# Optimization experiments

Measured on AMD Instinct MI355X. Metric: run time of the kernel, lower is better.

The kernel has to match this reference:

```python
import jax, jax.numpy as jnp
import numpy as np

N_P, N_D = 100000, 50000
C, S, H = 128, 128, 128
E = 600000


def setup_inputs() -> dict:
    key = jax.random.key(0)
    ks = jax.random.split(key, 20)
    sc = 1.0 / np.sqrt(H)
    inp = {
        "h_p": jax.random.normal(ks[0], (N_P, C), dtype=jnp.float32),
        "h_d": jax.random.normal(ks[1], (N_D, S), dtype=jnp.float32),
        "pd_src": jax.random.randint(ks[2], (E,), 0, N_P),
        "pd_dst": jax.random.randint(ks[3], (E,), 0, N_D),
        "dp_src": jax.random.randint(ks[4], (E,), 0, N_D),
        "dp_dst": jax.random.randint(ks[5], (E,), 0, N_P),
    }
    names = [("W1_pd", (C, H)), ("W1_dp", (S, H)), ("W2_pd", (H, H)),
             ("W2_dp", (H, H)), ("W3_pd", (H, S)), ("W3_dp", (H, C))]
    for i, (nm, shp) in enumerate(names):
        inp[nm] = jax.random.normal(ks[6 + i], shp, dtype=jnp.float32) * sc
        inp["b" + nm[1:]] = jnp.zeros((shp[1],), dtype=jnp.float32)
    return inp


def gconv(x, src, dst, n_dst, W, b):
    """DGL GraphConv, norm='both': relu(D_dst^-1/2 A D_src^-1/2 X W + b)."""
    n_src = x.shape[0]
    ones = jnp.ones(src.shape, dtype=x.dtype)
    deg_out = jnp.maximum(jax.ops.segment_sum(ones, src, num_segments=n_src), 1.0)
    deg_in = jnp.maximum(jax.ops.segment_sum(ones, dst, num_segments=n_dst), 1.0)
    xs = x * jax.lax.rsqrt(deg_out)[:, None]
    m = jax.ops.segment_sum(xs[src], dst, num_segments=n_dst)  # [n_dst, d_in]
    m = m * jax.lax.rsqrt(deg_in)[:, None]
    return jax.nn.relu(m @ W + b)


def reference(h_p, h_d, pd_src, pd_dst, dp_src, dp_dst,
              W1_pd, b1_pd, W1_dp, b1_dp,
              W2_pd, b2_pd, W2_dp, b2_dp,
              W3_pd, b3_pd, W3_dp, b3_dp):
    # Layer 1: p_d sends p feats to d; d_p sends d feats to p
    h_d1 = gconv(h_p, pd_src, pd_dst, N_D, W1_pd, b1_pd)
    h_p1 = gconv(h_d, dp_src, dp_dst, N_P, W1_dp, b1_dp)
    # Layer 2
    h_d2 = gconv(h_p1, pd_src, pd_dst, N_D, W2_pd, b2_pd)
    h_p2 = gconv(h_d1, dp_src, dp_dst, N_P, W2_dp, b2_dp)
    # Layer 3: d gets S-dim, p gets C-dim
    h_d3 = gconv(h_p2, pd_src, pd_dst, N_D, W3_pd, b3_pd)
    h_p3 = gconv(h_d2, dp_src, dp_dst, N_P, W3_dp, b3_dp)
    return h_p3, h_d3
```

## Files before the change

### kernel.cpp

```cpp
#include <hip/hip_runtime.h>
#include <stdint.h>

#define N_P 100000
#define N_D 50000
#define NE  600000
#define F   128
#define FP  136

#define NCHK   32
#define CHKE   18752
#define HPARTS 8
#define HPART_P (N_P/HPARTS)
#define HPART_D (N_D/HPARTS)
#define HOFS_A0 ((size_t)0)
#define HOFS_A1 ((size_t)32*N_P)
#define HOFS_A2 ((size_t)32*N_P + (size_t)32*N_D)
#define HOFS_A3 ((size_t)32*N_P + (size_t)64*N_D)

typedef __attribute__((ext_vector_type(8))) __bf16 bf16x8;
typedef __attribute__((ext_vector_type(4))) float  f32x4;

static __device__ __forceinline__ float bf2f(uint16_t u){
  union{float f;uint32_t i;} v; v.i = ((uint32_t)u)<<16; return v.f;
}
static __device__ __forceinline__ uint16_t f2bf(float f){
  union{float f;uint32_t i;} v; v.f = f;
  uint32_t i = v.i;
  uint32_t r = i + 0x7fffu + ((i>>16)&1u);
  return (uint16_t)(r>>16);
}

__global__ __launch_bounds__(256) void k_hist(
    const int* __restrict__ pd_src, const int* __restrict__ pd_dst,
    const int* __restrict__ dp_src, const int* __restrict__ dp_dst,
    int* __restrict__ hist){
  __shared__ int cnt[HPART_P];
  const int b = blockIdx.x;
  const int arr = b >> 8, part = (b >> 5) & 7, chunk = b & 31;
  const int* src; int N; size_t hofs;
  switch(arr){
    case 0:  src = pd_src; N = N_P; hofs = HOFS_A0; break;
    case 1:  src = pd_dst; N = N_D; hofs = HOFS_A1; break;
    case 2:  src = dp_src; N = N_D; hofs = HOFS_A2; break;
    default: src = dp_dst; N = N_P; hofs = HOFS_A3; break;
  }
  const int PART = N / HPARTS;
  const int lo = part * PART;
  for (int i = threadIdx.x; i < PART; i += 256) cnt[i] = 0;
  __syncthreads();
  const int e0 = chunk*CHKE, e1 = min(e0 + CHKE, NE);
  const uint4* s4 = (const uint4*)(src + e0);
  const int n4 = (e1 - e0) >> 2;
  for (int i = threadIdx.x; i < n4; i += 256){
    uint4 v = s4[i];
    int a0 = (int)v.x - lo, a1 = (int)v.y - lo, a2 = (int)v.z - lo, a3 = (int)v.w - lo;
    if ((unsigned)a0 < (unsigned)PART) atomicAdd(&cnt[a0], 1);
    if ((unsigned)a1 < (unsigned)PART) atomicAdd(&cnt[a1], 1);
    if ((unsigned)a2 < (unsigned)PART) atomicAdd(&cnt[a2], 1);
    if ((unsigned)a3 < (unsigned)PART) atomicAdd(&cnt[a3], 1);
  }
  __syncthreads();
  int* out = hist + hofs + (size_t)chunk*N + lo;
  for (int i = threadIdx.x; i < PART; i += 256) out[i] = cnt[i];
}

__global__ void k_sumdeg(int* __restrict__ hist,
                         int* __restrict__ cnt_d_in, int* __restrict__ cnt_p_in,
                         float* __restrict__ rs_p_out, float* __restrict__ rs_p_in,
                         float* __restrict__ rs_d_out, float* __restrict__ rs_d_in){
  const int idx = blockIdx.x*256 + threadIdx.x;
  const int arr = blockIdx.y;
  int N; size_t hofs; bool pre;
  switch(arr){
    case 0:  N = N_P; hofs = HOFS_A0; pre = false; break;
    case 1:  N = N_D; hofs = HOFS_A1; pre = true;  break;
    case 2:  N = N_D; hofs = HOFS_A2; pre = false; break;
    default: N = N_P; hofs = HOFS_A3; pre = true;  break;
  }
  if (idx >= N) return;
  int* base = hist + hofs + idx;
  int run = 0;
  if (pre){
    #pragma unroll 4
    for (int c = 0; c < NCHK; ++c){
      int v = base[(size_t)c*N]; base[(size_t)c*N] = run; run += v;
    }
  } else {
    #pragma unroll 4
    for (int c = 0; c < NCHK; ++c) run += base[(size_t)c*N];
  }
  float rs = rsqrtf((float)max(run, 1));
  switch(arr){
    case 0:  rs_p_out[idx] = rs; break;
    case 1:  cnt_d_in[idx] = run; rs_d_in[idx] = rs; break;
    case 2:  rs_d_out[idx] = rs; break;
    default: cnt_p_in[idx] = run; rs_p_in[idx] = rs; break;
  }
}

__global__ void k_scan1(const int* __restrict__ cA, int nA,
                        const int* __restrict__ cB, int nB,
                        int* __restrict__ bsums, int nbA){
  __shared__ int red[8];
  int b = blockIdx.x, t = threadIdx.x;
  const int* in; int n, bi, slot;
  if (b < nbA){ in = cA; n = nA; bi = b;       slot = bi; }
  else        { in = cB; n = nB; bi = b - nbA; slot = 256 + bi; }
  int i = bi*512 + t;
  int v = (i < n) ? in[i] : 0;
  #pragma unroll
  for (int o = 32; o; o >>= 1) v += __shfl_down(v, o, 64);
  if ((t & 63) == 0) red[t >> 6] = v;
  __syncthreads();
  if (t == 0){ int s = 0; for (int k = 0; k < 8; ++k) s += red[k]; bsums[slot] = s; }
}

__global__ void k_scan2(int* bsums, int nbA, int nbB){
  __shared__ int sh[256];
  int seg = blockIdx.x, t = threadIdx.x;
  int nb = seg ? nbB : nbA;
  int* p = bsums + seg*256;
  int v = (t < nb) ? p[t] : 0;
  sh[t] = v; __syncthreads();
  for (int ofs = 1; ofs < 256; ofs <<= 1){
    int u = (t >= ofs) ? sh[t-ofs] : 0; __syncthreads();
    sh[t] += u; __syncthreads();
  }
  if (t < nb) p[t] = sh[t] - v;
}

__global__ void k_scan3(const int* __restrict__ cA, int nA,
                        const int* __restrict__ cB, int nB,
                        const int* __restrict__ bsums, int nbA,
                        int* __restrict__ offA, int* __restrict__ offB){
  __shared__ int sh[512];
  int b = blockIdx.x, t = threadIdx.x;
  const int* in; int n, bi; int* out; int base;
  if (b < nbA){ in = cA; n = nA; bi = b;       out = offA; base = bsums[bi]; }
  else        { in = cB; n = nB; bi = b - nbA; out = offB; base = bsums[256+bi]; }
  int i = bi*512 + t;
  int v = (i < n) ? in[i] : 0;
  sh[t] = v; __syncthreads();
  for (int ofs = 1; ofs < 512; ofs <<= 1){
    int u = (t >= ofs) ? sh[t-ofs] : 0; __syncthreads();
    sh[t] += u; __syncthreads();
  }
  if (i < n) out[i] = base + sh[t] - v;
  if (b == 0 && t == 0){ offA[nA] = NE; offB[nB] = NE; }
}

__global__ __launch_bounds__(256) void k_scatter(
    const int* __restrict__ pd_src, const int* __restrict__ pd_dst,
    const int* __restrict__ dp_src, const int* __restrict__ dp_dst,
    const int* __restrict__ off_pd, const int* __restrict__ off_dp,
    const int* __restrict__ hist,
    int* __restrict__ col_pd, int* __restrict__ col_dp){
  __shared__ int base[HPART_P];
  const int b = blockIdx.x;
  const int gph = b >> 8, part = (b >> 5) & 7, chunk = b & 31;
  const int* dsts; const int* srcs; const int* off; int* col; int N; size_t hofs;
  if (gph == 0){ dsts = pd_dst; srcs = pd_src; off = off_pd; col = col_pd; N = N_D; hofs = HOFS_A1; }
  else         { dsts = dp_dst; srcs = dp_src; off = off_dp; col = col_dp; N = N_P; hofs = HOFS_A3; }
  const int PART = N / HPARTS;
  const int lo = part * PART;
  const int* hc   = hist + hofs + (size_t)chunk*N + lo;
  const int* offp = off + lo;
  for (int i = threadIdx.x; i < PART; i += 256) base[i] = offp[i] + hc[i];
  __syncthreads();
  const int e0 = chunk*CHKE, e1 = min(e0 + CHKE, NE);
  const uint4* d4 = (const uint4*)(dsts + e0);
  const int n4 = (e1 - e0) >> 2;
  for (int i = threadIdx.x; i < n4; i += 256){
    uint4 d = d4[i];
    int a0 = (int)d.x - lo, a1 = (int)d.y - lo, a2 = (int)d.z - lo, a3 = (int)d.w - lo;
    int e = e0 + 4*i;
    if ((unsigned)a0 < (unsigned)PART){ int p = atomicAdd(&base[a0], 1); col[p] = srcs[e+0]; }
    if ((unsigned)a1 < (unsigned)PART){ int p = atomicAdd(&base[a1], 1); col[p] = srcs[e+1]; }
    if ((unsigned)a2 < (unsigned)PART){ int p = atomicAdd(&base[a2], 1); col[p] = srcs[e+2]; }
    if ((unsigned)a3 < (unsigned)PART){ int p = atomicAdd(&base[a3], 1); col[p] = srcs[e+3]; }
  }
}

__global__ void k_convert(const float4* __restrict__ hp, const float4* __restrict__ hd,
                          const float* __restrict__ rs_po, const float* __restrict__ rs_do,
                          uint2* __restrict__ P0, uint2* __restrict__ D0,
                          const float* w0,const float* w1,const float* w2,
                          const float* w3,const float* w4,const float* w5,
                          uint16_t* __restrict__ wt,
                          uint16_t* z0, uint16_t* z1, uint16_t* z2,
                          uint16_t* z3, uint16_t* z4, uint16_t* z5){
  if (blockIdx.x < 6){
    int m = blockIdx.x;
    const float* W; uint16_t* Z;
    switch(m){ case 0:W=w0;Z=z0;break; case 1:W=w1;Z=z1;break; case 2:W=w2;Z=z2;break;
               case 3:W=w3;Z=z3;break; case 4:W=w4;Z=z4;break; default:W=w5;Z=z5; }
    uint16_t* T = wt + m*F*FP;
    for (int idx = threadIdx.x; idx < F*F; idx += 256){
      int k = idx >> 7, j = idx & 127;
      T[j*FP + k] = f2bf(W[idx]);
    }
    if (threadIdx.x < F) Z[threadIdx.x] = 0;
    return;
  }
  int i = (blockIdx.x - 6)*256 + threadIdx.x;
  const int nP4 = N_P*F/4, nD4 = N_D*F/4;
  if (i < nP4){
    float4 v = hp[i]; float s = rs_po[i >> 5];
    uint2 r;
    r.x = ((uint32_t)f2bf(v.y*s)<<16) | f2bf(v.x*s);
    r.y = ((uint32_t)f2bf(v.w*s)<<16) | f2bf(v.z*s);
    P0[i] = r;
  } else {
    int j = i - nP4;
    if (j < nD4){
      float4 v = hd[j]; float s = rs_do[j >> 5];
      uint2 r;
      r.x = ((uint32_t)f2bf(v.y*s)<<16) | f2bf(v.x*s);
      r.y = ((uint32_t)f2bf(v.w*s)<<16) | f2bf(v.z*s);
      D0[j] = r;
    }
  }
}

template<int OUT_MODE>
__global__ __launch_bounds__(256, 4) void k_gconv2(
    const uint16_t* __restrict__ xA, const int* __restrict__ offAp, const int* __restrict__ colA,
    const float* __restrict__ rsA, const uint16_t* __restrict__ WtA, const float* __restrict__ biasA,
    const float* __restrict__ rsnA, void* __restrict__ outA, int ndA, int nsA, int nblkA,
    const uint16_t* __restrict__ xB, const int* __restrict__ offBp, const int* __restrict__ colB,
    const float* __restrict__ rsB, const uint16_t* __restrict__ WtB, const float* __restrict__ biasB,
    const float* __restrict__ rsnB, void* __restrict__ outB, int ndB, int nsB)
{
  __shared__ uint16_t m_lds[64*FP];
  const int tid  = threadIdx.x;
  const int lane = tid & 63;
  const int wv   = tid >> 6;

  const uint16_t* x; const int* off; const int* col; const float* rs_in;
  const uint16_t* Wt; const float* bias; const float* rs_next; void* outp;
  int n_dst, zrow, bid;
  if ((int)blockIdx.x < nblkA){
    x = xA; off = offAp; col = colA; rs_in = rsA; Wt = WtA; bias = biasA;
    rs_next = rsnA; outp = outA; n_dst = ndA; zrow = nsA; bid = blockIdx.x;
  } else {
    x = xB; off = offBp; col = colB; rs_in = rsB; Wt = WtB; bias = biasB;
    rs_next = rsnB; outp = outB; n_dst = ndB; zrow = nsB; bid = blockIdx.x - nblkA;
  }

  const int row0 = bid*64 + wv*16;
  const int g    = lane >> 4;
  const int l    = lane & 15;
  const uint16_t* xl = x + l*8;

  int e0a[4], e1a[4], cva[4];
  #pragma unroll
  for (int i = 0; i < 4; ++i){
    int r = row0 + i*4 + g;
    bool rv = r < n_dst;
    e0a[i] = rv ? off[r]   : 0;
    e1a[i] = rv ? off[r+1] : 0;
  }
  #pragma unroll
  for (int i = 0; i < 4; ++i){
    int last = (e1a[i] > 0) ? e1a[i]-1 : 0;
    int idx  = e0a[i] + l;
    cva[i] = col[idx < e1a[i] ? idx : last];
  }

  #pragma unroll
  for (int i = 0; i < 4; ++i){
    int e0 = e0a[i], e1 = e1a[i];
    int cv = cva[i];
    float a0=0.f,a1=0.f,a2=0.f,a3=0.f,a4=0.f,a5=0.f,a6=0.f,a7=0.f;
    for (int e = e0; e < e1; e += 16){
      int nidx = e + 16 + l;
      int ncv  = col[nidx < e1 ? nidx : e1-1];
      int cnt  = e1 - e;
      const bool more = (cnt > 8);
      int cb[16];
      #pragma unroll
      for (int q = 0; q < 8; ++q) cb[q] = __shfl(cv, g*16 + q, 64);
      if (more){
        #pragma unroll
        for (int q = 8; q < 16; ++q) cb[q] = __shfl(cv, g*16 + q, 64);
      }
      uint4 u[8], w[8];
      #pragma unroll
      for (int q = 0; q < 8; ++q){
        int c = (q < cnt) ? cb[q] : zrow;
        u[q] = *(const uint4*)(xl + (size_t)c*F);
      }
      if (more){
        #pragma unroll
        for (int q = 8; q < 16; ++q){
          int c = (q < cnt) ? cb[q] : zrow;
          w[q-8] = *(const uint4*)(xl + (size_t)c*F);
        }
      }
      #pragma unroll
      for (int q = 0; q < 8; ++q){
        a0 += bf2f((uint16_t)u[q].x); a1 += bf2f((uint16_t)(u[q].x>>16));
        a2 += bf2f((uint16_t)u[q].y); a3 += bf2f((uint16_t)(u[q].y>>16));
        a4 += bf2f((uint16_t)u[q].z); a5 += bf2f((uint16_t)(u[q].z>>16));
        a6 += bf2f((uint16_t)u[q].w); a7 += bf2f((uint16_t)(u[q].w>>16));
      }
      if (more){
        #pragma unroll
        for (int q = 0; q < 8; ++q){
          a0 += bf2f((uint16_t)w[q].x); a1 += bf2f((uint16_t)(w[q].x>>16));
          a2 += bf2f((uint16_t)w[q].y); a3 += bf2f((uint16_t)(w[q].y>>16));
          a4 += bf2f((uint16_t)w[q].z); a5 += bf2f((uint16_t)(w[q].z>>16));
          a6 += bf2f((uint16_t)w[q].w); a7 += bf2f((uint16_t)(w[q].w>>16));
        }
      }
      cv = ncv;
    }
    int r = row0 + i*4 + g;
    float rs = (r < n_dst) ? rs_in[r] : 0.f;
    uint4 pk;
    pk.x = ((uint32_t)f2bf(a1*rs)<<16) | f2bf(a0*rs);
    pk.y = ((uint32_t)f2bf(a3*rs)<<16) | f2bf(a2*rs);
    pk.z = ((uint32_t)f2bf(a5*rs)<<16) | f2bf(a4*rs);
    pk.w = ((uint32_t)f2bf(a7*rs)<<16) | f2bf(a6*rs);
    *(uint4*)&m_lds[(wv*16 + i*4 + g)*FP + l*8] = pk;
  }

  f32x4 acc[8];
  #pragma unroll
  for (int t = 0; t < 8; ++t) acc[t] = (f32x4){0.f,0.f,0.f,0.f};
  const int mrow = lane & 15;
  const int kgrp = lane >> 4;
  #pragma unroll
  for (int k0 = 0; k0 < F; k0 += 32){
    bf16x8 bfrag = *(const bf16x8*)&m_lds[(wv*16 + mrow)*FP + k0 + kgrp*8];
    #pragma unroll
    for (int t = 0; t < 8; ++t){
      bf16x8 afrag = *(const bf16x8*)&Wt[(t*16 + mrow)*FP + k0 + kgrp*8];
      acc[t] = __builtin_amdgcn_mfma_f32_16x16x32_bf16(afrag, bfrag, acc[t], 0, 0, 0);
    }
  }

  const int q4 = kgrp * 4;
  const int rr = row0 + mrow;
  if (rr < n_dst){
    float rsn = (OUT_MODE == 0) ? rs_next[rr] : 1.f;
    #pragma unroll
    for (int t = 0; t < 8; ++t){
      float4 b4 = *(const float4*)&bias[t*16 + q4];
      float v0 = fmaxf(acc[t][0] + b4.x, 0.f);
      float v1 = fmaxf(acc[t][1] + b4.y, 0.f);
      float v2 = fmaxf(acc[t][2] + b4.z, 0.f);
      float v3 = fmaxf(acc[t][3] + b4.w, 0.f);
      if (OUT_MODE == 0){
        uint2 pk;
        pk.x = ((uint32_t)f2bf(v1*rsn)<<16) | f2bf(v0*rsn);
        pk.y = ((uint32_t)f2bf(v3*rsn)<<16) | f2bf(v2*rsn);
        *(uint2*)((uint16_t*)outp + (size_t)rr*F + t*16 + q4) = pk;
      } else {
        float4 o; o.x = v0; o.y = v1; o.z = v2; o.w = v3;
        *(float4*)((float*)outp + (size_t)rr*F + t*16 + q4) = o;
      }
    }
  }
}

extern "C" void kernel_launch(void* const* d_in, const int* in_sizes, int n_in,
                              void* d_out, int out_size, void* d_ws, size_t ws_size,
                              hipStream_t stream) {
  const float* h_p   = (const float*)d_in[0];
  const float* h_d   = (const float*)d_in[1];
  const int* pd_src  = (const int*)d_in[2];
  const int* pd_dst  = (const int*)d_in[3];
  const int* dp_src  = (const int*)d_in[4];
  const int* dp_dst  = (const int*)d_in[5];
  const float* W1_pd = (const float*)d_in[6];   const float* b1_pd = (const float*)d_in[7];
  const float* W1_dp = (const float*)d_in[8];   const float* b1_dp = (const float*)d_in[9];
  const float* W2_pd = (const float*)d_in[10];  const float* b2_pd = (const float*)d_in[11];
  const float* W2_dp = (const float*)d_in[12];  const float* b2_dp = (const float*)d_in[13];
  const float* W3_pd = (const float*)d_in[14];  const float* b3_pd = (const float*)d_in[15];
  const float* W3_dp = (const float*)d_in[16];  const float* b3_dp = (const float*)d_in[17];

  char* w = (char*)d_ws;
  size_t o = 0;
  auto take = [&](size_t bytes)->char*{
    char* p = w + o; o += (bytes + 255) & ~(size_t)255; return p;
  };

  int* cnt_d_in  = (int*)take(4*(size_t)N_D);
  int* cnt_p_in  = (int*)take(4*(size_t)N_P);
  int* off_pd   = (int*)take(4*(size_t)(N_D+1));
  int* off_dp   = (int*)take(4*(size_t)(N_P+1));
  int* bsums    = (int*)take(4*512);
  int* col_pd   = (int*)take(4*(size_t)NE);
  int* col_dp   = (int*)take(4*(size_t)NE);
  float* rs_p_out = (float*)take(4*(size_t)N_P);
  float* rs_p_in  = (float*)take(4*(size_t)N_P);
  float* rs_d_out = (float*)take(4*(size_t)N_D);
  float* rs_d_in  = (float*)take(4*(size_t)N_D);
  uint16_t* wt  = (uint16_t*)take(2*(size_t)6*F*FP);
  uint16_t* P0  = (uint16_t*)take(2*(size_t)(N_P+1)*F);
  uint16_t* P1  = (uint16_t*)take(2*(size_t)(N_P+1)*F);
  uint16_t* P2  = (uint16_t*)take(2*(size_t)(N_P+1)*F);
  uint16_t* D0  = (uint16_t*)take(2*(size_t)(N_D+1)*F);
  uint16_t* D1  = (uint16_t*)take(2*(size_t)(N_D+1)*F);
  uint16_t* D2  = (uint16_t*)take(2*(size_t)(N_D+1)*F);

  int* hist = (int*)P1;

  k_hist<<<4*HPARTS*NCHK, 256, 0, stream>>>(pd_src, pd_dst, dp_src, dp_dst, hist);
  k_sumdeg<<<dim3((N_P+255)/256, 4), 256, 0, stream>>>(
      hist, cnt_d_in, cnt_p_in, rs_p_out, rs_p_in, rs_d_out, rs_d_in);
  const int nbA = (N_D + 511)/512;
  const int nbB = (N_P + 511)/512;
  k_scan1<<<nbA+nbB, 512, 0, stream>>>(cnt_d_in, N_D, cnt_p_in, N_P, bsums, nbA);
  k_scan2<<<2, 256, 0, stream>>>(bsums, nbA, nbB);
  k_scan3<<<nbA+nbB, 512, 0, stream>>>(cnt_d_in, N_D, cnt_p_in, N_P, bsums, nbA, off_pd, off_dp);
  k_scatter<<<2*HPARTS*NCHK, 256, 0, stream>>>(pd_src, pd_dst, dp_src, dp_dst,
                                               off_pd, off_dp, hist, col_pd, col_dp);
  k_convert<<<((N_P+N_D)*F/4 + 255)/256 + 6, 256, 0, stream>>>(
      (const float4*)h_p, (const float4*)h_d, rs_p_out, rs_d_out, (uint2*)P0, (uint2*)D0,
      W1_pd, W1_dp, W2_pd, W2_dp, W3_pd, W3_dp, wt,
      P0 + (size_t)N_P*F, D0 + (size_t)N_D*F,
      P1 + (size_t)N_P*F, D1 + (size_t)N_D*F,
      P2 + (size_t)N_P*F, D2 + (size_t)N_D*F);

  const int gd = (N_D + 63)/64, gp = (N_P + 63)/64;
  k_gconv2<0><<<gd+gp, 256, 0, stream>>>(
      P0, off_pd, col_pd, rs_d_in, wt + 0*F*FP, b1_pd, rs_d_out, D1, N_D, N_P, gd,
      D0, off_dp, col_dp, rs_p_in, wt + 1*F*FP, b1_dp, rs_p_out, P1, N_P, N_D);
  k_gconv2<0><<<gd+gp, 256, 0, stream>>>(
      P1, off_pd, col_pd, rs_d_in, wt + 2*F*FP, b2_pd, rs_d_out, D2, N_D, N_P, gd,
      D1, off_dp, col_dp, rs_p_in, wt + 3*F*FP, b2_dp, rs_p_out, P2, N_P, N_D);
  k_gconv2<1><<<gd+gp, 256, 0, stream>>>(
      P2, off_pd, col_pd, rs_d_in, wt + 4*F*FP, b3_pd, nullptr, (float*)d_out + (size_t)N_P*F, N_D, N_P, gd,
      D2, off_dp, col_dp, rs_p_in, wt + 5*F*FP, b3_dp, nullptr, (float*)d_out, N_P, N_D);
}
```

Before: 465.8 us.

## Interleave two destination rows with software-pipelined 8-edge gather chunks

Restructures the gather-aggregate loop so that two destination rows are processed at once. Each row works through 8-edge chunks, and the loads for the next chunk are issued before the current chunk is accumulated. This is meant to raise memory-level parallelism and hide gather latency, since the old loop loaded and consumed each 16-edge chunk serially. The cost is more registers (two sets of 8 uint4 buffers plus accumulators), which could lower occupancy, and rows with uneven degree leave some iterations doing work for only one of the pair.

```diff
diff --git a/kernel.cpp b/kernel.cpp
--- a/kernel.cpp
+++ b/kernel.cpp
@@ -250,6 +250,7 @@
   const int row0 = bid*64 + wv*16;
   const int g    = lane >> 4;
   const int l    = lane & 15;
+  const int l8   = lane & 7;
   const uint16_t* xl = x + l*8;
 
   int e0a[4], e1a[4], cva[4];
@@ -262,67 +263,98 @@
   }
   #pragma unroll
   for (int i = 0; i < 4; ++i){
-    int last = (e1a[i] > 0) ? e1a[i]-1 : 0;
-    int idx  = e0a[i] + l;
-    cva[i] = col[idx < e1a[i] ? idx : last];
-  }
-
-  #pragma unroll
-  for (int i = 0; i < 4; ++i){
-    int e0 = e0a[i], e1 = e1a[i];
-    int cv = cva[i];
-    float a0=0.f,a1=0.f,a2=0.f,a3=0.f,a4=0.f,a5=0.f,a6=0.f,a7=0.f;
-    for (int e = e0; e < e1; e += 16){
-      int nidx = e + 16 + l;
-      int ncv  = col[nidx < e1 ? nidx : e1-1];
-      int cnt  = e1 - e;
-      const bool more = (cnt > 8);
-      int cb[16];
-      #pragma unroll
-      for (int q = 0; q < 8; ++q) cb[q] = __shfl(cv, g*16 + q, 64);
-      if (more){
+    int idx = e0a[i] + l8;
+    cva[i] = col[idx < e1a[i] ? idx : (e1a[i] > 0 ? e1a[i]-1 : 0)];
+  }
+
+  #pragma unroll
+  for (int pr = 0; pr < 2; ++pr){
+    const int iA = 2*pr, iB = 2*pr + 1;
+    int eA = e0a[iA]; const int e1A = e1a[iA];
+    int eB = e0a[iB]; const int e1B = e1a[iB];
+    int cvA = cva[iA], cvB = cva[iB];
+    float aA[8], aB[8];
+    #pragma unroll
+    for (int q = 0; q < 8; ++q){ aA[q] = 0.f; aB[q] = 0.f; }
+    uint4 uA[8], uB[8];
+
+    int cntA = e1A - eA; cntA = cntA > 8 ? 8 : (cntA < 0 ? 0 : cntA);
+    #pragma unroll
+    for (int q = 0; q < 8; ++q){
+      int c = (q < cntA) ? __shfl(cvA, g*16 + q, 64) : zrow;
+      uA[q] = *(const uint4*)(xl + (size_t)c*F);
+    }
+    { int nidx = eA + 8 + l8; cvA = col[nidx < e1A ? nidx : (e1A > 0 ? e1A-1 : 0)]; }
+
+    int cntB = e1B - eB; cntB = cntB > 8 ? 8 : (cntB < 0 ? 0 : cntB);
+    #pragma unroll
+    for (int q = 0; q < 8; ++q){
+      int c = (q < cntB) ? __shfl(cvB, g*16 + q, 64) : zrow;
+      uB[q] = *(const uint4*)(xl + (size_t)c*F);
+    }
+    { int nidx = eB + 8 + l8; cvB = col[nidx < e1B ? nidx : (e1B > 0 ? e1B-1 : 0)]; }
+
+    while (cntA | cntB){
+      if (cntA){
         #pragma unroll
-        for (int q = 8; q < 16; ++q) cb[q] = __shfl(cv, g*16 + q, 64);
-      }
-      uint4 u[8], w[8];
-      #pragma unroll
-      for (int q = 0; q < 8; ++q){
-        int c = (q < cnt) ? cb[q] : zrow;
-        u[q] = *(const uint4*)(xl + (size_t)c*F);
-      }
-      if (more){
-        #pragma unroll
-        for (int q = 8; q < 16; ++q){
-          int c = (q < cnt) ? cb[q] : zrow;
-          w[q-8] = *(const uint4*)(xl + (size_t)c*F);
+        for (int q = 0; q < 8; ++q){
+          aA[0] += bf2f((uint16_t)uA[q].x); aA[1] += bf2f((uint16_t)(uA[q].x>>16));
+          aA[2] += bf2f((uint16_t)uA[q].y); aA[3] += bf2f((uint16_t)(uA[q].y>>16));
+          aA[4] += bf2f((uint16_t)uA[q].z); aA[5] += bf2f((uint16_t)(uA[q].z>>16));
+          aA[6] += bf2f((uint16_t)uA[q].w); aA[7] += bf2f((uint16_t)(uA[q].w>>16));
+        }
+        eA += cntA;
+        cntA = e1A - eA; cntA = cntA > 8 ? 8 : (cntA < 0 ? 0 : cntA);
+        if (cntA){
+          #pragma unroll
+          for (int q = 0; q < 8; ++q){
+            int c = (q < cntA) ? __shfl(cvA, g*16 + q, 64) : zrow;
+            uA[q] = *(const uint4*)(xl + (size_t)c*F);
+          }
+          int nidx = eA + 8 + l8; cvA = col[nidx < e1A ? nidx : e1A-1];
         }
       }
-      #pragma unroll
-      for (int q = 0; q < 8; ++q){
-        a0 += bf2f((uint16_t)u[q].x); a1 += bf2f((uint16_t)(u[q].x>>16));
-        a2 += bf2f((uint16_t)u[q].y); a3 += bf2f((uint16_t)(u[q].y>>16));
-        a4 += bf2f((uint16_t)u[q].z); a5 += bf2f((uint16_t)(u[q].z>>16));
-        a6 += bf2f((uint16_t)u[q].w); a7 += bf2f((uint16_t)(u[q].w>>16));
-      }
-      if (more){
+      if (cntB){
         #pragma unroll
         for (int q = 0; q < 8; ++q){
-          a0 += bf2f((uint16_t)w[q].x); a1 += bf2f((uint16_t)(w[q].x>>16));
-          a2 += bf2f((uint16_t)w[q].y); a3 += bf2f((uint16_t)(w[q].y>>16));
-          a4 += bf2f((uint16_t)w[q].z); a5 += bf2f((uint16_t)(w[q].z>>16));
-          a6 += bf2f((uint16_t)w[q].w); a7 += bf2f((uint16_t)(w[q].w>>16));
+          aB[0] += bf2f((uint16_t)uB[q].x); aB[1] += bf2f((uint16_t)(uB[q].x>>16));
+          aB[2] += bf2f((uint16_t)uB[q].y); aB[3] += bf2f((uint16_t)(uB[q].y>>16));
+          aB[4] += bf2f((uint16_t)uB[q].z); aB[5] += bf2f((uint16_t)(uB[q].z>>16));
+          aB[6] += bf2f((uint16_t)uB[q].w); aB[7] += bf2f((uint16_t)(uB[q].w>>16));
+        }
+        eB += cntB;
+        cntB = e1B - eB; cntB = cntB > 8 ? 8 : (cntB < 0 ? 0 : cntB);
+        if (cntB){
+          #pragma unroll
+          for (int q = 0; q < 8; ++q){
+            int c = (q < cntB) ? __shfl(cvB, g*16 + q, 64) : zrow;
+            uB[q] = *(const uint4*)(xl + (size_t)c*F);
+          }
+          int nidx = eB + 8 + l8; cvB = col[nidx < e1B ? nidx : e1B-1];
         }
       }
-      cv = ncv;
-    }
-    int r = row0 + i*4 + g;
-    float rs = (r < n_dst) ? rs_in[r] : 0.f;
-    uint4 pk;
-    pk.x = ((uint32_t)f2bf(a1*rs)<<16) | f2bf(a0*rs);
-    pk.y = ((uint32_t)f2bf(a3*rs)<<16) | f2bf(a2*rs);
-    pk.z = ((uint32_t)f2bf(a5*rs)<<16) | f2bf(a4*rs);
-    pk.w = ((uint32_t)f2bf(a7*rs)<<16) | f2bf(a6*rs);
-    *(uint4*)&m_lds[(wv*16 + i*4 + g)*FP + l*8] = pk;
+    }
+
+    {
+      int r = row0 + iA*4 + g;
+      float rs = (r < n_dst) ? rs_in[r] : 0.f;
+      uint4 pk;
+      pk.x = ((uint32_t)f2bf(aA[1]*rs)<<16) | f2bf(aA[0]*rs);
+      pk.y = ((uint32_t)f2bf(aA[3]*rs)<<16) | f2bf(aA[2]*rs);
+      pk.z = ((uint32_t)f2bf(aA[5]*rs)<<16) | f2bf(aA[4]*rs);
+      pk.w = ((uint32_t)f2bf(aA[7]*rs)<<16) | f2bf(aA[6]*rs);
+      *(uint4*)&m_lds[(wv*16 + iA*4 + g)*FP + l*8] = pk;
+    }
+    {
+      int r = row0 + iB*4 + g;
+      float rs = (r < n_dst) ? rs_in[r] : 0.f;
+      uint4 pk;
+      pk.x = ((uint32_t)f2bf(aB[1]*rs)<<16) | f2bf(aB[0]*rs);
+      pk.y = ((uint32_t)f2bf(aB[3]*rs)<<16) | f2bf(aB[2]*rs);
+      pk.z = ((uint32_t)f2bf(aB[5]*rs)<<16) | f2bf(aB[4]*rs);
+      pk.w = ((uint32_t)f2bf(aB[7]*rs)<<16) | f2bf(aB[6]*rs);
+      *(uint4*)&m_lds[(wv*16 + iB*4 + g)*FP + l*8] = pk;
+    }
   }
 
   f32x4 acc[8];
```

New measurement: 514.3 us. 10.4% more time.

## Replace chunked LDS histogram CSR build with global-atomic degree count and scatter

Applied to the files above, without the earlier changes.

Degree counting now uses direct global atomics on zeroed degree arrays instead of per-chunk shared-memory histograms plus a column-summing pass, and the rsqrt normalisation moves into the first scan kernel. The CSR scatter likewise uses global atomic cursors initialised by the scan rather than per-block LDS bases from the histogram. This removes the large histogram buffer traffic and the many redundant edge re-reads per partition, at the cost of global atomic contention and a non-deterministic edge order within each row.

```diff
diff --git a/kernel.cpp b/kernel.cpp
--- a/kernel.cpp
+++ b/kernel.cpp
@@ -7,16 +7,6 @@
 #define F   128
 #define FP  136
 
-#define NCHK   32
-#define CHKE   18752
-#define HPARTS 8
-#define HPART_P (N_P/HPARTS)
-#define HPART_D (N_D/HPARTS)
-#define HOFS_A0 ((size_t)0)
-#define HOFS_A1 ((size_t)32*N_P)
-#define HOFS_A2 ((size_t)32*N_P + (size_t)32*N_D)
-#define HOFS_A3 ((size_t)32*N_P + (size_t)64*N_D)
-
 typedef __attribute__((ext_vector_type(8))) __bf16 bf16x8;
 typedef __attribute__((ext_vector_type(4))) float  f32x4;
 
@@ -30,89 +20,54 @@
   return (uint16_t)(r>>16);
 }
 
-__global__ __launch_bounds__(256) void k_hist(
+__global__ __launch_bounds__(256) void k_deg(
     const int* __restrict__ pd_src, const int* __restrict__ pd_dst,
     const int* __restrict__ dp_src, const int* __restrict__ dp_dst,
-    int* __restrict__ hist){
-  __shared__ int cnt[HPART_P];
-  const int b = blockIdx.x;
-  const int arr = b >> 8, part = (b >> 5) & 7, chunk = b & 31;
-  const int* src; int N; size_t hofs;
+    int* __restrict__ deg_p_out, int* __restrict__ deg_d_in,
+    int* __restrict__ deg_d_out, int* __restrict__ deg_p_in){
+  const int n4 = NE/4;
+  int i = blockIdx.x*256 + threadIdx.x;
+  if (i >= 4*n4) return;
+  const int arr = i / n4;
+  const int j   = i - arr*n4;
+  const uint4* s4; int* deg;
   switch(arr){
-    case 0:  src = pd_src; N = N_P; hofs = HOFS_A0; break;
-    case 1:  src = pd_dst; N = N_D; hofs = HOFS_A1; break;
-    case 2:  src = dp_src; N = N_D; hofs = HOFS_A2; break;
-    default: src = dp_dst; N = N_P; hofs = HOFS_A3; break;
-  }
-  const int PART = N / HPARTS;
-  const int lo = part * PART;
-  for (int i = threadIdx.x; i < PART; i += 256) cnt[i] = 0;
-  __syncthreads();
-  const int e0 = chunk*CHKE, e1 = min(e0 + CHKE, NE);
-  const uint4* s4 = (const uint4*)(src + e0);
-  const int n4 = (e1 - e0) >> 2;
-  for (int i = threadIdx.x; i < n4; i += 256){
-    uint4 v = s4[i];
-    int a0 = (int)v.x - lo, a1 = (int)v.y - lo, a2 = (int)v.z - lo, a3 = (int)v.w - lo;
-    if ((unsigned)a0 < (unsigned)PART) atomicAdd(&cnt[a0], 1);
-    if ((unsigned)a1 < (unsigned)PART) atomicAdd(&cnt[a1], 1);
-    if ((unsigned)a2 < (unsigned)PART) atomicAdd(&cnt[a2], 1);
-    if ((unsigned)a3 < (unsigned)PART) atomicAdd(&cnt[a3], 1);
-  }
-  __syncthreads();
-  int* out = hist + hofs + (size_t)chunk*N + lo;
-  for (int i = threadIdx.x; i < PART; i += 256) out[i] = cnt[i];
-}
-
-__global__ void k_sumdeg(int* __restrict__ hist,
-                         int* __restrict__ cnt_d_in, int* __restrict__ cnt_p_in,
-                         float* __restrict__ rs_p_out, float* __restrict__ rs_p_in,
-                         float* __restrict__ rs_d_out, float* __restrict__ rs_d_in){
-  const int idx = blockIdx.x*256 + threadIdx.x;
-  const int arr = blockIdx.y;
-  int N; size_t hofs; bool pre;
-  switch(arr){
-    case 0:  N = N_P; hofs = HOFS_A0; pre = false; break;
-    case 1:  N = N_D; hofs = HOFS_A1; pre = true;  break;
-    case 2:  N = N_D; hofs = HOFS_A2; pre = false; break;
-    default: N = N_P; hofs = HOFS_A3; pre = true;  break;
-  }
-  if (idx >= N) return;
-  int* base = hist + hofs + idx;
-  int run = 0;
-  if (pre){
-    #pragma unroll 4
-    for (int c = 0; c < NCHK; ++c){
-      int v = base[(size_t)c*N]; base[(size_t)c*N] = run; run += v;
-    }
-  } else {
-    #pragma unroll 4
-    for (int c = 0; c < NCHK; ++c) run += base[(size_t)c*N];
-  }
-  float rs = rsqrtf((float)max(run, 1));
-  switch(arr){
-    case 0:  rs_p_out[idx] = rs; break;
-    case 1:  cnt_d_in[idx] = run; rs_d_in[idx] = rs; break;
-    case 2:  rs_d_out[idx] = rs; break;
-    default: cnt_p_in[idx] = run; rs_p_in[idx] = rs; break;
-  }
+    case 0:  s4 = (const uint4*)pd_src; deg = deg_p_out; break;
+    case 1:  s4 = (const uint4*)pd_dst; deg = deg_d_in;  break;
+    case 2:  s4 = (const uint4*)dp_src; deg = deg_d_out; break;
+    default: s4 = (const uint4*)dp_dst; deg = deg_p_in;  break;
+  }
+  uint4 v = s4[j];
+  atomicAdd(&deg[v.x], 1);
+  atomicAdd(&deg[v.y], 1);
+  atomicAdd(&deg[v.z], 1);
+  atomicAdd(&deg[v.w], 1);
 }
 
 __global__ void k_scan1(const int* __restrict__ cA, int nA,
                         const int* __restrict__ cB, int nB,
-                        int* __restrict__ bsums, int nbA){
+                        int* __restrict__ bsums, int nbA,
+                        const int* __restrict__ oA, const int* __restrict__ oB,
+                        float* __restrict__ riA, float* __restrict__ roA,
+                        float* __restrict__ riB, float* __restrict__ roB){
   __shared__ int red[8];
   int b = blockIdx.x, t = threadIdx.x;
-  const int* in; int n, bi, slot;
-  if (b < nbA){ in = cA; n = nA; bi = b;       slot = bi; }
-  else        { in = cB; n = nB; bi = b - nbA; slot = 256 + bi; }
+  const int* in; const int* od; float* ri; float* ro; int n, bi, slot;
+  if (b < nbA){ in = cA; od = oA; ri = riA; ro = roA; n = nA; bi = b;       slot = bi; }
+  else        { in = cB; od = oB; ri = riB; ro = roB; n = nB; bi = b - nbA; slot = 256 + bi; }
   int i = bi*512 + t;
-  int v = (i < n) ? in[i] : 0;
-  #pragma unroll
-  for (int o = 32; o; o >>= 1) v += __shfl_down(v, o, 64);
-  if ((t & 63) == 0) red[t >> 6] = v;
+  int v = 0;
+  if (i < n){
+    v = in[i];
+    ri[i] = rsqrtf((float)max(v, 1));
+    ro[i] = rsqrtf((float)max(od[i], 1));
+  }
+  int s = v;
+  #pragma unroll
+  for (int o = 32; o; o >>= 1) s += __shfl_down(s, o, 64);
+  if ((t & 63) == 0) red[t >> 6] = s;
   __syncthreads();
-  if (t == 0){ int s = 0; for (int k = 0; k < 8; ++k) s += red[k]; bsums[slot] = s; }
+  if (t == 0){ int acc = 0; for (int k = 0; k < 8; ++k) acc += red[k]; bsums[slot] = acc; }
 }
 
 __global__ void k_scan2(int* bsums, int nbA, int nbB){
@@ -132,12 +87,13 @@
 __global__ void k_scan3(const int* __restrict__ cA, int nA,
                         const int* __restrict__ cB, int nB,
                         const int* __restrict__ bsums, int nbA,
-                        int* __restrict__ offA, int* __restrict__ offB){
+                        int* __restrict__ offA, int* __restrict__ offB,
+                        int* __restrict__ curA, int* __restrict__ curB){
   __shared__ int sh[512];
   int b = blockIdx.x, t = threadIdx.x;
-  const int* in; int n, bi; int* out; int base;
-  if (b < nbA){ in = cA; n = nA; bi = b;       out = offA; base = bsums[bi]; }
-  else        { in = cB; n = nB; bi = b - nbA; out = offB; base = bsums[256+bi]; }
+  const int* in; int n, bi; int* out; int* cur; int base;
+  if (b < nbA){ in = cA; n = nA; bi = b;       out = offA; cur = curA; base = bsums[bi]; }
+  else        { in = cB; n = nB; bi = b - nbA; out = offB; cur = curB; base = bsums[256+bi]; }
   int i = bi*512 + t;
   int v = (i < n) ? in[i] : 0;
   sh[t] = v; __syncthreads();
@@ -145,40 +101,28 @@
     int u = (t >= ofs) ? sh[t-ofs] : 0; __syncthreads();
     sh[t] += u; __syncthreads();
   }
-  if (i < n) out[i] = base + sh[t] - v;
+  if (i < n){ int val = base + sh[t] - v; out[i] = val; cur[i] = val; }
   if (b == 0 && t == 0){ offA[nA] = NE; offB[nB] = NE; }
 }
 
-__global__ __launch_bounds__(256) void k_scatter(
+__global__ __launch_bounds__(256) void k_scatter2(
     const int* __restrict__ pd_src, const int* __restrict__ pd_dst,
     const int* __restrict__ dp_src, const int* __restrict__ dp_dst,
-    const int* __restrict__ off_pd, const int* __restrict__ off_dp,
-    const int* __restrict__ hist,
+    int* __restrict__ cur_pd, int* __restrict__ cur_dp,
     int* __restrict__ col_pd, int* __restrict__ col_dp){
-  __shared__ int base[HPART_P];
-  const int b = blockIdx.x;
-  const int gph = b >> 8, part = (b >> 5) & 7, chunk = b & 31;
-  const int* dsts; const int* srcs; const int* off; int* col; int N; size_t hofs;
-  if (gph == 0){ dsts = pd_dst; srcs = pd_src; off = off_pd; col = col_pd; N = N_D; hofs = HOFS_A1; }
-  else         { dsts = dp_dst; srcs = dp_src; off = off_dp; col = col_dp; N = N_P; hofs = HOFS_A3; }
-  const int PART = N / HPARTS;
-  const int lo = part * PART;
-  const int* hc   = hist + hofs + (size_t)chunk*N + lo;
-  const int* offp = off + lo;
-  for (int i = threadIdx.x; i < PART; i += 256) base[i] = offp[i] + hc[i];
-  __syncthreads();
-  const int e0 = chunk*CHKE, e1 = min(e0 + CHKE, NE);
-  const uint4* d4 = (const uint4*)(dsts + e0);
-  const int n4 = (e1 - e0) >> 2;
-  for (int i = threadIdx.x; i < n4; i += 256){
-    uint4 d = d4[i];
-    int a0 = (int)d.x - lo, a1 = (int)d.y - lo, a2 = (int)d.z - lo, a3 = (int)d.w - lo;
-    int e = e0 + 4*i;
-    if ((unsigned)a0 < (unsigned)PART){ int p = atomicAdd(&base[a0], 1); col[p] = srcs[e+0]; }
-    if ((unsigned)a1 < (unsigned)PART){ int p = atomicAdd(&base[a1], 1); col[p] = srcs[e+1]; }
-    if ((unsigned)a2 < (unsigned)PART){ int p = atomicAdd(&base[a2], 1); col[p] = srcs[e+2]; }
-    if ((unsigned)a3 < (unsigned)PART){ int p = atomicAdd(&base[a3], 1); col[p] = srcs[e+3]; }
-  }
+  const int n4 = NE/4;
+  int i = blockIdx.x*256 + threadIdx.x;
+  if (i >= 2*n4) return;
+  const int* srcs; const int* dsts; int* cur; int* col; int j;
+  if (i < n4){ srcs = pd_src; dsts = pd_dst; cur = cur_pd; col = col_pd; j = i; }
+  else       { srcs = dp_src; dsts = dp_dst; cur = cur_dp; col = col_dp; j = i - n4; }
+  uint4 d = ((const uint4*)dsts)[j];
+  uint4 s = ((const uint4*)srcs)[j];
+  int p;
+  p = atomicAdd(&cur[d.x], 1); col[p] = s.x;
+  p = atomicAdd(&cur[d.y], 1); col[p] = s.y;
+  p = atomicAdd(&cur[d.z], 1); col[p] = s.z;
+  p = atomicAdd(&cur[d.w], 1); col[p] = s.w;
 }
 
 __global__ void k_convert(const float4* __restrict__ hp, const float4* __restrict__ hd,
@@ -386,10 +330,16 @@
     char* p = w + o; o += (bytes + 255) & ~(size_t)255; return p;
   };
 
-  int* cnt_d_in  = (int*)take(4*(size_t)N_D);
-  int* cnt_p_in  = (int*)take(4*(size_t)N_P);
+  int* degblock  = (int*)take(4*(size_t)(2*N_D + 2*N_P));
+  int* cnt_d_in  = degblock;
+  int* cnt_p_in  = degblock + N_D;
+  int* deg_d_out = degblock + N_D + N_P;
+  int* deg_p_out = degblock + 2*N_D + N_P;
+
   int* off_pd   = (int*)take(4*(size_t)(N_D+1));
   int* off_dp   = (int*)take(4*(size_t)(N_P+1));
+  int* cur_pd   = (int*)take(4*(size_t)N_D);
+  int* cur_dp   = (int*)take(4*(size_t)N_P);
   int* bsums    = (int*)take(4*512);
   int* col_pd   = (int*)take(4*(size_t)NE);
   int* col_dp   = (int*)take(4*(size_t)NE);
@@ -405,18 +355,19 @@
   uint16_t* D1  = (uint16_t*)take(2*(size_t)(N_D+1)*F);
   uint16_t* D2  = (uint16_t*)take(2*(size_t)(N_D+1)*F);
 
-  int* hist = (int*)P1;
-
-  k_hist<<<4*HPARTS*NCHK, 256, 0, stream>>>(pd_src, pd_dst, dp_src, dp_dst, hist);
-  k_sumdeg<<<dim3((N_P+255)/256, 4), 256, 0, stream>>>(
-      hist, cnt_d_in, cnt_p_in, rs_p_out, rs_p_in, rs_d_out, rs_d_in);
+  hipMemsetAsync(degblock, 0, 4*(size_t)(2*N_D + 2*N_P), stream);
+  k_deg<<<(NE + 255)/256, 256, 0, stream>>>(pd_src, pd_dst, dp_src, dp_dst,
+                                            deg_p_out, cnt_d_in, deg_d_out, cnt_p_in);
   const int nbA = (N_D + 511)/512;
   const int nbB = (N_P + 511)/512;
-  k_scan1<<<nbA+nbB, 512, 0, stream>>>(cnt_d_in, N_D, cnt_p_in, N_P, bsums, nbA);
+  k_scan1<<<nbA+nbB, 512, 0, stream>>>(cnt_d_in, N_D, cnt_p_in, N_P, bsums, nbA,
+                                       deg_d_out, deg_p_out,
+                                       rs_d_in, rs_d_out, rs_p_in, rs_p_out);
   k_scan2<<<2, 256, 0, stream>>>(bsums, nbA, nbB);
-  k_scan3<<<nbA+nbB, 512, 0, stream>>>(cnt_d_in, N_D, cnt_p_in, N_P, bsums, nbA, off_pd, off_dp);
-  k_scatter<<<2*HPARTS*NCHK, 256, 0, stream>>>(pd_src, pd_dst, dp_src, dp_dst,
-                                               off_pd, off_dp, hist, col_pd, col_dp);
+  k_scan3<<<nbA+nbB, 512, 0, stream>>>(cnt_d_in, N_D, cnt_p_in, N_P, bsums, nbA,
+                                       off_pd, off_dp, cur_pd, cur_dp);
+  k_scatter2<<<(2*(NE/4) + 255)/256, 256, 0, stream>>>(
+      pd_src, pd_dst, dp_src, dp_dst, cur_pd, cur_dp, col_pd, col_dp);
   k_convert<<<((N_P+N_D)*F/4 + 255)/256 + 6, 256, 0, stream>>>(
       (const float4*)h_p, (const float4*)h_d, rs_p_out, rs_d_out, (uint2*)P0, (uint2*)D0,
       W1_pd, W1_dp, W2_pd, W2_dp, W3_pd, W3_dp, wt,
```

Measured after the change: 561.1 us. 20.5% more time.

## Pack 16-bit histogram counters in LDS and halve edge chunks

Applied to the files above, without the earlier changes.

The histogram kernel now packs two 16-bit counters into each 32-bit LDS word. Each block can then cover a quarter of the node range instead of an eighth. The number of edge chunks is halved from 32 to 16 and both the histogram and scatter kernels move to 512-thread blocks. This cuts the number of blocks that each rescan the edge arrays and shrinks the per-chunk histogram written to global memory. The cost is fewer, larger blocks with more LDS each, and it relies on per-chunk counts staying below 65536.

```diff
diff --git a/kernel.cpp b/kernel.cpp
--- a/kernel.cpp
+++ b/kernel.cpp
@@ -7,15 +7,14 @@
 #define F   128
 #define FP  136
 
-#define NCHK   32
-#define CHKE   18752
-#define HPARTS 8
-#define HPART_P (N_P/HPARTS)
-#define HPART_D (N_D/HPARTS)
+#define NCHK   16
+#define CHKE   37504
+#define HPH    4
+#define HPS    8
 #define HOFS_A0 ((size_t)0)
-#define HOFS_A1 ((size_t)32*N_P)
-#define HOFS_A2 ((size_t)32*N_P + (size_t)32*N_D)
-#define HOFS_A3 ((size_t)32*N_P + (size_t)64*N_D)
+#define HOFS_A1 ((size_t)NCHK*N_P)
+#define HOFS_A2 ((size_t)NCHK*N_P + (size_t)NCHK*N_D)
+#define HOFS_A3 ((size_t)NCHK*N_P + (size_t)2*NCHK*N_D)
 
 typedef __attribute__((ext_vector_type(8))) __bf16 bf16x8;
 typedef __attribute__((ext_vector_type(4))) float  f32x4;
@@ -30,13 +29,13 @@
   return (uint16_t)(r>>16);
 }
 
-__global__ __launch_bounds__(256) void k_hist(
+__global__ __launch_bounds__(512) void k_hist(
     const int* __restrict__ pd_src, const int* __restrict__ pd_dst,
     const int* __restrict__ dp_src, const int* __restrict__ dp_dst,
     int* __restrict__ hist){
-  __shared__ int cnt[HPART_P];
+  __shared__ uint32_t cnt[(N_P/HPH)/2];
   const int b = blockIdx.x;
-  const int arr = b >> 8, part = (b >> 5) & 7, chunk = b & 31;
+  const int arr = b >> 6, part = (b >> 4) & 3, chunk = b & 15;
   const int* src; int N; size_t hofs;
   switch(arr){
     case 0:  src = pd_src; N = N_P; hofs = HOFS_A0; break;
@@ -44,24 +43,29 @@
     case 2:  src = dp_src; N = N_D; hofs = HOFS_A2; break;
     default: src = dp_dst; N = N_P; hofs = HOFS_A3; break;
   }
-  const int PART = N / HPARTS;
-  const int lo = part * PART;
-  for (int i = threadIdx.x; i < PART; i += 256) cnt[i] = 0;
+  const int PART = N / HPH;
+  const int nw   = PART >> 1;
+  const int lo   = part * PART;
+  for (int i = threadIdx.x; i < nw; i += 512) cnt[i] = 0;
   __syncthreads();
   const int e0 = chunk*CHKE, e1 = min(e0 + CHKE, NE);
   const uint4* s4 = (const uint4*)(src + e0);
   const int n4 = (e1 - e0) >> 2;
-  for (int i = threadIdx.x; i < n4; i += 256){
+  for (int i = threadIdx.x; i < n4; i += 512){
     uint4 v = s4[i];
     int a0 = (int)v.x - lo, a1 = (int)v.y - lo, a2 = (int)v.z - lo, a3 = (int)v.w - lo;
-    if ((unsigned)a0 < (unsigned)PART) atomicAdd(&cnt[a0], 1);
-    if ((unsigned)a1 < (unsigned)PART) atomicAdd(&cnt[a1], 1);
-    if ((unsigned)a2 < (unsigned)PART) atomicAdd(&cnt[a2], 1);
-    if ((unsigned)a3 < (unsigned)PART) atomicAdd(&cnt[a3], 1);
+    if ((unsigned)a0 < (unsigned)PART) atomicAdd(&cnt[a0>>1], 1u << ((a0&1)<<4));
+    if ((unsigned)a1 < (unsigned)PART) atomicAdd(&cnt[a1>>1], 1u << ((a1&1)<<4));
+    if ((unsigned)a2 < (unsigned)PART) atomicAdd(&cnt[a2>>1], 1u << ((a2&1)<<4));
+    if ((unsigned)a3 < (unsigned)PART) atomicAdd(&cnt[a3>>1], 1u << ((a3&1)<<4));
   }
   __syncthreads();
   int* out = hist + hofs + (size_t)chunk*N + lo;
-  for (int i = threadIdx.x; i < PART; i += 256) out[i] = cnt[i];
+  for (int i = threadIdx.x; i < nw; i += 512){
+    uint32_t w = cnt[i];
+    out[2*i]   = (int)(w & 0xffffu);
+    out[2*i+1] = (int)(w >> 16);
+  }
 }
 
 __global__ void k_sumdeg(int* __restrict__ hist,
@@ -149,28 +153,28 @@
   if (b == 0 && t == 0){ offA[nA] = NE; offB[nB] = NE; }
 }
 
-__global__ __launch_bounds__(256) void k_scatter(
+__global__ __launch_bounds__(512) void k_scatter(
     const int* __restrict__ pd_src, const int* __restrict__ pd_dst,
     const int* __restrict__ dp_src, const int* __restrict__ dp_dst,
     const int* __restrict__ off_pd, const int* __restrict__ off_dp,
     const int* __restrict__ hist,
     int* __restrict__ col_pd, int* __restrict__ col_dp){
-  __shared__ int base[HPART_P];
+  __shared__ int base[N_P/HPS];
   const int b = blockIdx.x;
-  const int gph = b >> 8, part = (b >> 5) & 7, chunk = b & 31;
+  const int gph = b >> 7, part = (b >> 4) & 7, chunk = b & 15;
   const int* dsts; const int* srcs; const int* off; int* col; int N; size_t hofs;
   if (gph == 0){ dsts = pd_dst; srcs = pd_src; off = off_pd; col = col_pd; N = N_D; hofs = HOFS_A1; }
   else         { dsts = dp_dst; srcs = dp_src; off = off_dp; col = col_dp; N = N_P; hofs = HOFS_A3; }
-  const int PART = N / HPARTS;
+  const int PART = N / HPS;
   const int lo = part * PART;
   const int* hc   = hist + hofs + (size_t)chunk*N + lo;
   const int* offp = off + lo;
-  for (int i = threadIdx.x; i < PART; i += 256) base[i] = offp[i] + hc[i];
+  for (int i = threadIdx.x; i < PART; i += 512) base[i] = offp[i] + hc[i];
   __syncthreads();
   const int e0 = chunk*CHKE, e1 = min(e0 + CHKE, NE);
   const uint4* d4 = (const uint4*)(dsts + e0);
   const int n4 = (e1 - e0) >> 2;
-  for (int i = threadIdx.x; i < n4; i += 256){
+  for (int i = threadIdx.x; i < n4; i += 512){
     uint4 d = d4[i];
     int a0 = (int)d.x - lo, a1 = (int)d.y - lo, a2 = (int)d.z - lo, a3 = (int)d.w - lo;
     int e = e0 + 4*i;
@@ -407,7 +411,7 @@
 
   int* hist = (int*)P1;
 
-  k_hist<<<4*HPARTS*NCHK, 256, 0, stream>>>(pd_src, pd_dst, dp_src, dp_dst, hist);
+  k_hist<<<4*HPH*NCHK, 512, 0, stream>>>(pd_src, pd_dst, dp_src, dp_dst, hist);
   k_sumdeg<<<dim3((N_P+255)/256, 4), 256, 0, stream>>>(
       hist, cnt_d_in, cnt_p_in, rs_p_out, rs_p_in, rs_d_out, rs_d_in);
   const int nbA = (N_D + 511)/512;
@@ -415,8 +419,8 @@
   k_scan1<<<nbA+nbB, 512, 0, stream>>>(cnt_d_in, N_D, cnt_p_in, N_P, bsums, nbA);
   k_scan2<<<2, 256, 0, stream>>>(bsums, nbA, nbB);
   k_scan3<<<nbA+nbB, 512, 0, stream>>>(cnt_d_in, N_D, cnt_p_in, N_P, bsums, nbA, off_pd, off_dp);
-  k_scatter<<<2*HPARTS*NCHK, 256, 0, stream>>>(pd_src, pd_dst, dp_src, dp_dst,
-                                               off_pd, off_dp, hist, col_pd, col_dp);
+  k_scatter<<<2*HPS*NCHK, 512, 0, stream>>>(pd_src, pd_dst, dp_src, dp_dst,
+                                            off_pd, off_dp, hist, col_pd, col_dp);
   k_convert<<<((N_P+N_D)*F/4 + 255)/256 + 6, 256, 0, stream>>>(
       (const float4*)h_p, (const float4*)h_d, rs_p_out, rs_d_out, (uint2*)P0, (uint2*)D0,
       W1_pd, W1_dp, W2_pd, W2_dp, W3_pd, W3_dp, wt,
```

Result: faster. 446.9 us (-4.1%).
